# Kernel optimization log

Measured on AMD Instinct MI355X. Metric: run time of the kernel, lower is better.

Reference implementation:

```python
import jax, jax.numpy as jnp
import numpy as np

B, T, I, H, L, O = 256, 256, 512, 1024, 2, 1


def setup_inputs() -> dict:
    key = jax.random.key(0)
    ks = jax.random.split(key, 8)
    s_i = 1.0 / np.sqrt(I)
    s_h = 1.0 / np.sqrt(H)
    return {
        "init_hidden": jax.random.normal(ks[0], (B, H), jnp.float32),
        "context": jax.random.normal(ks[1], (B, T, I), jnp.float32),
        "W_ih0": jax.random.normal(ks[2], (4 * H, I), jnp.float32) * s_i,
        "W_hh0": jax.random.normal(ks[3], (4 * H, H), jnp.float32) * s_h,
        "b_ih0": jnp.zeros((4 * H,), jnp.float32),
        "b_hh0": jnp.zeros((4 * H,), jnp.float32),
        "W_ih1": jax.random.normal(ks[4], (4 * H, H), jnp.float32) * s_h,
        "W_hh1": jax.random.normal(ks[5], (4 * H, H), jnp.float32) * s_h,
        "b_ih1": jnp.zeros((4 * H,), jnp.float32),
        "b_hh1": jnp.zeros((4 * H,), jnp.float32),
        "W_ro": jax.random.normal(ks[6], (O, H), jnp.float32) * s_h,
        "b_ro": jnp.zeros((O,), jnp.float32),
    }


def _lstm_layer(x, h0, c0, W_ih, W_hh, b_ih, b_hh):
    """x: [B,T,Din] -> all hidden states [B,T,H]. PyTorch gate order i,f,g,o."""
    # Precompute input contribution for all timesteps (one big GEMM).
    xg = jnp.einsum('btd,gd->btg', x, W_ih) + b_ih + b_hh  # [B,T,4H]

    def step(carry, xg_t):
        h, c = carry
        gates = xg_t + h @ W_hh.T                          # [B,4H]
        i, f, g, o = jnp.split(gates, 4, axis=-1)
        i = jax.nn.sigmoid(i)
        f = jax.nn.sigmoid(f)
        g = jnp.tanh(g)
        o = jax.nn.sigmoid(o)
        c = f * c + i * g
        h = o * jnp.tanh(c)
        return (h, c), h

    (_, _), hs = jax.lax.scan(step, (h0, c0), jnp.swapaxes(xg, 0, 1))
    return jnp.swapaxes(hs, 0, 1)  # [B,T,H]


def reference(init_hidden, context, W_ih0, W_hh0, b_ih0, b_hh0,
              W_ih1, W_hh1, b_ih1, b_hh1, W_ro, b_ro):
    c0 = jnp.zeros((context.shape[0], H), context.dtype)
    # h0 for every layer is the same init_hidden (torch.stack of init_hidden).
    h1 = _lstm_layer(context, init_hidden, c0, W_ih0, W_hh0, b_ih0, b_hh0)
    h2 = _lstm_layer(h1, init_hidden, c0, W_ih1, W_hh1, b_ih1, b_hh1)
    # readout on last timestep -> [B, O]
    return h2[:, -1, :] @ W_ro.T + b_ro
```

## Files before the change

kernel.cpp:

```cpp
#include <hip/hip_runtime.h>
#include <hip/hip_bf16.h>

#define B_ 256
#define T_ 256
#define I_ 512
#define H_ 1024
#define CH 8
#define NCH 32

typedef _Float16 half8 __attribute__((ext_vector_type(8)));
typedef float floatx4 __attribute__((ext_vector_type(4)));


__global__ __launch_bounds__(256) void prep_w(
    _Float16* __restrict__ dst, const float* __restrict__ src, int K) {
  const int np = blockIdx.y;
  const int k = blockIdx.x * 256 + threadIdx.x;
  const int cc = np & 63, g = cc >> 4, j = cc & 15;
  const int orig = g * H_ + (np >> 6) * 16 + j;
  dst[(size_t)np * K + k] = (_Float16)src[(size_t)orig * K + k];
}

__global__ __launch_bounds__(256) void prep_bias(
    float* __restrict__ bs0, float* __restrict__ bs1,
    const float* __restrict__ bih0, const float* __restrict__ bhh0,
    const float* __restrict__ bih1, const float* __restrict__ bhh1) {
  const int np = blockIdx.x * 256 + threadIdx.x;
  const int cc = np & 63, g = cc >> 4, j = cc & 15;
  const int orig = g * H_ + (np >> 6) * 16 + j;
  bs0[np] = bih0[orig] + bhh0[orig];
  bs1[np] = bih1[orig] + bhh1[orig];
}

__global__ __launch_bounds__(256) void prep_state(
    const float* __restrict__ init, _Float16* __restrict__ h1s,
    _Float16* __restrict__ h2s, float* __restrict__ c0, float* __restrict__ c1) {
  const int idx = blockIdx.x * 256 + threadIdx.x;
  const float v = init[idx];
  h1s[B_ * H_ + idx] = (_Float16)v;
  h2s[B_ * H_ + idx] = (_Float16)v;
  c0[idx] = 0.f;
  c1[idx] = 0.f;
}

template<int KK, int AMODE>
__global__ __launch_bounds__(256, 2) void gemm_xg(
    const void* __restrict__ Ap, const _Float16* __restrict__ Bw,
    const float* __restrict__ bias, _Float16* __restrict__ out, int tbase) {
  constexpr int NST = KK / 64;
  __shared__ _Float16 As[2][128 * 72];
  __shared__ _Float16 Bs[2][128 * 72];
  const int tid = threadIdx.x;
  const int row0 = blockIdx.x * 128, col0 = blockIdx.y * 128;
  const int sr = tid >> 1, sc = (tid & 1) * 32;
  const int gr = row0 + sr;
  const size_t arow = (AMODE == 0)
      ? ((size_t)(gr & 255) * T_ + (size_t)tbase + (gr >> 8)) * I_
      : (size_t)gr * KK;
  const float*    af32 = (const float*)Ap + arow + sc;
  const _Float16* af16 = (const _Float16*)Ap + arow + sc;
  const _Float16* bsrc = Bw + (size_t)(col0 + sr) * KK + sc;

  const int w = tid >> 6, lane = tid & 63;
  const int wm = (w >> 1) * 64, wn = (w & 1) * 64;
  const int l15 = lane & 15, kg = (lane >> 4) * 8;
  floatx4 acc[4][4] = {};
  half8 ar[4], br[4];

  auto load_stage = [&](int ki) {
    const int k = ki * 64;
    #pragma unroll
    for (int c = 0; c < 4; ++c) {
      if (AMODE == 0) {
        float4 f0 = *(const float4*)(af32 + k + c * 8);
        float4 f1 = *(const float4*)(af32 + k + c * 8 + 4);
        half8 h;
        h[0] = (_Float16)f0.x; h[1] = (_Float16)f0.y;
        h[2] = (_Float16)f0.z; h[3] = (_Float16)f0.w;
        h[4] = (_Float16)f1.x; h[5] = (_Float16)f1.y;
        h[6] = (_Float16)f1.z; h[7] = (_Float16)f1.w;
        ar[c] = h;
      } else {
        ar[c] = *(const half8*)(af16 + k + c * 8);
      }
      br[c] = *(const half8*)(bsrc + k + c * 8);
    }
  };
  auto write_stage = [&](int buf) {
    #pragma unroll
    for (int c = 0; c < 4; ++c) *(half8*)(&As[buf][sr * 72 + sc + c * 8]) = ar[c];
    #pragma unroll
    for (int c = 0; c < 4; ++c) *(half8*)(&Bs[buf][sr * 72 + sc + c * 8]) = br[c];
  };

  load_stage(0); write_stage(0); __syncthreads();
  for (int ki = 0; ki < NST; ++ki) {
    const int cur = ki & 1;
    if (ki + 1 < NST) load_stage(ki + 1);
    #pragma unroll
    for (int ks = 0; ks < 2; ++ks) {
      half8 bf[4];
      #pragma unroll
      for (int n = 0; n < 4; ++n)
        bf[n] = *(const half8*)(&Bs[cur][(wn + 16 * n + l15) * 72 + ks * 32 + kg]);
      #pragma unroll
      for (int m = 0; m < 4; ++m) {
        half8 af = *(const half8*)(&As[cur][(wm + 16 * m + l15) * 72 + ks * 32 + kg]);
        #pragma unroll
        for (int n = 0; n < 4; ++n)
          acc[m][n] = __builtin_amdgcn_mfma_f32_16x16x32_f16(af, bf[n], acc[m][n], 0, 0, 0);
      }
    }
    if (ki + 1 < NST) write_stage(cur ^ 1);
    __syncthreads();
  }

  const int crow = (lane >> 4) * 4;
  #pragma unroll
  for (int n = 0; n < 4; ++n) {
    const int col = col0 + wn + 16 * n + l15;
    const float bv = bias[col];
    #pragma unroll
    for (int m = 0; m < 4; ++m) {
      const int rbase = row0 + wm + 16 * m + crow;
      #pragma unroll
      for (int r = 0; r < 4; ++r)
        out[(size_t)(rbase + r) * 4096 + col] = (_Float16)(acc[m][n][r] + bv);
    }
  }
}

__global__ __launch_bounds__(256, 2) void lstm_step(
    const _Float16* __restrict__ Wh0, const _Float16* __restrict__ Wh1,
    const _Float16* __restrict__ xg0, const _Float16* __restrict__ xg1,
    _Float16* __restrict__ h1s, _Float16* __restrict__ h2s,
    _Float16* __restrict__ h1chunk, float* __restrict__ c0buf,
    float* __restrict__ c1buf, float* __restrict__ hF, int t0, int t1, int ci) {
  const int layer = blockIdx.x >> 8;
  const int t = layer ? t1 : t0;
  if (t < 0) return;
  const int tb = blockIdx.x & 255;
  const int row0 = (tb >> 6) * 64;
  const int nb = tb & 63;
  const int col0 = nb * 64;
  const _Float16* __restrict__ Wh = layer ? Wh1 : Wh0;
  const _Float16* __restrict__ xg = (layer ? xg1 : xg0) + (size_t)ci * 256 * 4096;
  _Float16* __restrict__ hs = layer ? h2s : h1s;
  float* __restrict__ cbuf = layer ? c1buf : c0buf;
  const int rd = (t + 1) & 1, wr = t & 1;
  const _Float16* __restrict__ hin = hs + rd * (B_ * H_);

  __shared__ _Float16 lds[2 * (2 * 2 * 64 * 72)];
  _Float16* As = lds;
  _Float16* Bs = lds + 2 * 2 * 64 * 72;
  float* gl = (float*)lds;

  const int tid = threadIdx.x;
  const int sr = tid >> 2, kh_s = (tid >> 1) & 1, coff = (tid & 1) * 32;
  const _Float16* asrc = hin + (size_t)(row0 + sr) * H_ + kh_s * 512 + coff;
  const _Float16* bsrc = Wh + (size_t)(col0 + sr) * H_ + kh_s * 512 + coff;
  const int sdst = kh_s * (64 * 72) + sr * 72 + coff;

  const int w = tid >> 6, lane = tid & 63;
  const int rh = (w & 1) * 32, kh = w >> 1;
  const int l15 = lane & 15, kg = (lane >> 4) * 8;
  floatx4 acc[2][4] = {};
  half8 ar[4], br[4];

  auto load_stage = [&](int ki) {
    #pragma unroll
    for (int c = 0; c < 4; ++c) ar[c] = *(const half8*)(asrc + ki * 64 + c * 8);
    #pragma unroll
    for (int c = 0; c < 4; ++c) br[c] = *(const half8*)(bsrc + ki * 64 + c * 8);
  };
  auto write_stage = [&](int buf) {
    _Float16* dA = As + buf * (2 * 64 * 72) + sdst;
    _Float16* dB = Bs + buf * (2 * 64 * 72) + sdst;
    #pragma unroll
    for (int c = 0; c < 4; ++c) *(half8*)(dA + c * 8) = ar[c];
    #pragma unroll
    for (int c = 0; c < 4; ++c) *(half8*)(dB + c * 8) = br[c];
  };

  load_stage(0); write_stage(0); __syncthreads();
  for (int ki = 0; ki < 8; ++ki) {
    const int cur = ki & 1;
    if (ki < 7) load_stage(ki + 1);
    const _Float16* Ab = As + cur * (2 * 64 * 72) + kh * (64 * 72);
    const _Float16* Bb = Bs + cur * (2 * 64 * 72) + kh * (64 * 72);
    #pragma unroll
    for (int ks = 0; ks < 2; ++ks) {
      half8 bf[4];
      #pragma unroll
      for (int n = 0; n < 4; ++n)
        bf[n] = *(const half8*)(Bb + (16 * n + l15) * 72 + ks * 32 + kg);
      #pragma unroll
      for (int m = 0; m < 2; ++m) {
        half8 af = *(const half8*)(Ab + (rh + 16 * m + l15) * 72 + ks * 32 + kg);
        #pragma unroll
        for (int n = 0; n < 4; ++n)
          acc[m][n] = __builtin_amdgcn_mfma_f32_16x16x32_f16(af, bf[n], acc[m][n], 0, 0, 0);
      }
    }
    if (ki < 7) write_stage(cur ^ 1);
    __syncthreads();
  }

  const int crow = (lane >> 4) * 4;
  if (kh == 0) {
    #pragma unroll
    for (int m = 0; m < 2; ++m)
      #pragma unroll
      for (int n = 0; n < 4; ++n) {
        const int col = 16 * n + l15, rowl = rh + 16 * m + crow;
        #pragma unroll
        for (int r = 0; r < 4; ++r) gl[(rowl + r) * 68 + col] = acc[m][n][r];
      }
  }
  __syncthreads();
  if (kh == 1) {
    #pragma unroll
    for (int m = 0; m < 2; ++m)
      #pragma unroll
      for (int n = 0; n < 4; ++n) {
        const int col = 16 * n + l15, rowl = rh + 16 * m + crow;
        #pragma unroll
        for (int r = 0; r < 4; ++r) gl[(rowl + r) * 68 + col] += acc[m][n][r];
      }
  }
  __syncthreads();

  #pragma unroll
  for (int q = 0; q < 4; ++q) {
    const int idx = tid + q * 256;
    const int r = idx >> 4, j = idx & 15;
    const int brow = row0 + r;
    const int hu = nb * 16 + j;
    const _Float16* xr = xg + (size_t)brow * 4096 + col0;
    float gi = gl[r * 68 + j]          + (float)xr[j];
    float gf = gl[r * 68 + 16 + j]     + (float)xr[16 + j];
    float gg = gl[r * 68 + 32 + j]     + (float)xr[32 + j];
    float go = gl[r * 68 + 48 + j]     + (float)xr[48 + j];
    const float si = 1.f / (1.f + expf(-gi));
    const float sf = 1.f / (1.f + expf(-gf));
    const float so = 1.f / (1.f + expf(-go));
    const float tg = tanhf(gg);
    const float cp = cbuf[(size_t)brow * H_ + hu];
    const float cn = sf * cp + si * tg;
    const float hn = so * tanhf(cn);
    cbuf[(size_t)brow * H_ + hu] = cn;
    hs[wr * (B_ * H_) + (size_t)brow * H_ + hu] = (_Float16)hn;
    if (layer == 0)
      h1chunk[((size_t)ci * 256 + brow) * H_ + hu] = (_Float16)hn;
    else
      hF[(size_t)brow * H_ + hu] = hn;
  }
}

__global__ __launch_bounds__(256) void readout(
    const float* __restrict__ hF, const float* __restrict__ Wro,
    const float* __restrict__ bro, float* __restrict__ out) {
  const int b = blockIdx.x;
  const int tid = threadIdx.x;
  float p = 0.f;
  for (int h = tid; h < H_; h += 256) p += hF[(size_t)b * H_ + h] * Wro[h];
  #pragma unroll
  for (int off = 32; off; off >>= 1) p += __shfl_down(p, off, 64);
  __shared__ float red[4];
  if ((tid & 63) == 0) red[tid >> 6] = p;
  __syncthreads();
  if (tid == 0) out[b] = red[0] + red[1] + red[2] + red[3] + bro[0];
}

extern "C" void kernel_launch(void* const* d_in, const int* in_sizes, int n_in,
                              void* d_out, int out_size, void* d_ws, size_t ws_size,
                              hipStream_t stream) {
  const float* init_hidden = (const float*)d_in[0];
  const float* ctx   = (const float*)d_in[1];
  const float* W_ih0 = (const float*)d_in[2];
  const float* W_hh0 = (const float*)d_in[3];
  const float* b_ih0 = (const float*)d_in[4];
  const float* b_hh0 = (const float*)d_in[5];
  const float* W_ih1 = (const float*)d_in[6];
  const float* W_hh1 = (const float*)d_in[7];
  const float* b_ih1 = (const float*)d_in[8];
  const float* b_hh1 = (const float*)d_in[9];
  const float* W_ro  = (const float*)d_in[10];
  const float* b_ro  = (const float*)d_in[11];

  char* ws = (char*)d_ws;
  _Float16* W0p  = (_Float16*)(ws);
  _Float16* Wh0p = (_Float16*)(ws + 4194304);
  _Float16* W1p  = (_Float16*)(ws + 12582912);
  _Float16* Wh1p = (_Float16*)(ws + 20971520);
  float*    bs0  = (float*)(ws + 29360128);
  float*    bs1  = (float*)(ws + 29376512);
  _Float16* xg0  = (_Float16*)(ws + 29392896);
  _Float16* xg1  = (_Float16*)(ws + 46170112);
  _Float16* h1c  = (_Float16*)(ws + 62947328);
  _Float16* h1s  = (_Float16*)(ws + 67141632);
  _Float16* h2s  = (_Float16*)(ws + 68190208);
  float*    c0   = (float*)(ws + 69238784);
  float*    c1   = (float*)(ws + 70287360);
  float*    hF   = (float*)(ws + 71335936);

  prep_w<<<dim3(I_ / 256, 4096), 256, 0, stream>>>(W0p, W_ih0, I_);
  prep_w<<<dim3(H_ / 256, 4096), 256, 0, stream>>>(Wh0p, W_hh0, H_);
  prep_w<<<dim3(H_ / 256, 4096), 256, 0, stream>>>(W1p, W_ih1, H_);
  prep_w<<<dim3(H_ / 256, 4096), 256, 0, stream>>>(Wh1p, W_hh1, H_);
  prep_bias<<<dim3(16), 256, 0, stream>>>(bs0, bs1, b_ih0, b_hh0, b_ih1, b_hh1);
  prep_state<<<dim3(B_ * H_ / 256), 256, 0, stream>>>(init_hidden, h1s, h2s, c0, c1);

  for (int c = 0; c <= NCH; ++c) {
    if (c < NCH)
      gemm_xg<512, 0><<<dim3(16, 32), 256, 0, stream>>>(ctx, W0p, bs0, xg0, c * CH);
    if (c >= 1)
      gemm_xg<1024, 1><<<dim3(16, 32), 256, 0, stream>>>(h1c, W1p, bs1, xg1, 0);
    for (int i = 0; i < CH; ++i) {
      const int t0 = (c < NCH) ? c * CH + i : -1;
      const int t1 = (c >= 1) ? (c - 1) * CH + i : -1;
      lstm_step<<<dim3(512), 256, 0, stream>>>(Wh0p, Wh1p, xg0, xg1, h1s, h2s,
                                               h1c, c0, c1, hF, t0, t1, i);
    }
  }
  readout<<<dim3(B_), 256, 0, stream>>>(hF, W_ro, b_ro, (float*)d_out);
}
```

Baseline: 5.971 ms.

## Enlarge LSTM step tiles to full-K 128-row blocks and use fast activations

Measured after the change: 6.533 ms. 1.09x slower.

```diff
diff --git a/kernel.cpp b/kernel.cpp
--- a/kernel.cpp
+++ b/kernel.cpp
@@ -10,6 +10,13 @@
 
 typedef _Float16 half8 __attribute__((ext_vector_type(8)));
 typedef float floatx4 __attribute__((ext_vector_type(4)));
+
+__device__ __forceinline__ float fsig(float x) {
+  return 1.f / (1.f + __expf(-x));
+}
+__device__ __forceinline__ float ftanh(float x) {
+  return 1.f - 2.f / (__expf(2.f * x) + 1.f);
+}
 
 
 __global__ __launch_bounds__(256) void prep_w(
@@ -130,18 +137,19 @@
   }
 }
 
-__global__ __launch_bounds__(256, 2) void lstm_step(
+__global__ __launch_bounds__(256) void lstm_step(
     const _Float16* __restrict__ Wh0, const _Float16* __restrict__ Wh1,
     const _Float16* __restrict__ xg0, const _Float16* __restrict__ xg1,
     _Float16* __restrict__ h1s, _Float16* __restrict__ h2s,
     _Float16* __restrict__ h1chunk, float* __restrict__ c0buf,
     float* __restrict__ c1buf, float* __restrict__ hF, int t0, int t1, int ci) {
-  const int layer = blockIdx.x >> 8;
+  const int bid = blockIdx.x;
+  const int layer = bid >> 7;
   const int t = layer ? t1 : t0;
   if (t < 0) return;
-  const int tb = blockIdx.x & 255;
-  const int row0 = (tb >> 6) * 64;
-  const int nb = tb & 63;
+  const int b7 = bid & 127;
+  const int row0 = (b7 >> 6) * 128;
+  const int nb = b7 & 63;
   const int col0 = nb * 64;
   const _Float16* __restrict__ Wh = layer ? Wh1 : Wh0;
   const _Float16* __restrict__ xg = (layer ? xg1 : xg0) + (size_t)ci * 256 * 4096;
@@ -150,110 +158,83 @@
   const int rd = (t + 1) & 1, wr = t & 1;
   const _Float16* __restrict__ hin = hs + rd * (B_ * H_);
 
-  __shared__ _Float16 lds[2 * (2 * 2 * 64 * 72)];
-  _Float16* As = lds;
-  _Float16* Bs = lds + 2 * 2 * 64 * 72;
-  float* gl = (float*)lds;
+  __shared__ _Float16 As[2][128 * 72];
+  __shared__ _Float16 Bs[2][64 * 72];
 
   const int tid = threadIdx.x;
-  const int sr = tid >> 2, kh_s = (tid >> 1) & 1, coff = (tid & 1) * 32;
-  const _Float16* asrc = hin + (size_t)(row0 + sr) * H_ + kh_s * 512 + coff;
-  const _Float16* bsrc = Wh + (size_t)(col0 + sr) * H_ + kh_s * 512 + coff;
-  const int sdst = kh_s * (64 * 72) + sr * 72 + coff;
-
-  const int w = tid >> 6, lane = tid & 63;
-  const int rh = (w & 1) * 32, kh = w >> 1;
-  const int l15 = lane & 15, kg = (lane >> 4) * 8;
-  floatx4 acc[2][4] = {};
-  half8 ar[4], br[4];
+  const int srow = tid >> 3;
+  const int spc = (tid & 7) * 8;
+  const _Float16* asrc = hin + (size_t)(row0 + srow) * H_ + spc;
+  const _Float16* bsrc = Wh + (size_t)(col0 + srow) * H_ + spc;
+  half8 ar[4], br[2];
 
   auto load_stage = [&](int ki) {
-    #pragma unroll
-    for (int c = 0; c < 4; ++c) ar[c] = *(const half8*)(asrc + ki * 64 + c * 8);
-    #pragma unroll
-    for (int c = 0; c < 4; ++c) br[c] = *(const half8*)(bsrc + ki * 64 + c * 8);
+    const int k = ki * 64;
+    #pragma unroll
+    for (int p = 0; p < 4; ++p) ar[p] = *(const half8*)(asrc + (size_t)(p * 32) * H_ + k);
+    #pragma unroll
+    for (int p = 0; p < 2; ++p) br[p] = *(const half8*)(bsrc + (size_t)(p * 32) * H_ + k);
   };
   auto write_stage = [&](int buf) {
-    _Float16* dA = As + buf * (2 * 64 * 72) + sdst;
-    _Float16* dB = Bs + buf * (2 * 64 * 72) + sdst;
-    #pragma unroll
-    for (int c = 0; c < 4; ++c) *(half8*)(dA + c * 8) = ar[c];
-    #pragma unroll
-    for (int c = 0; c < 4; ++c) *(half8*)(dB + c * 8) = br[c];
+    #pragma unroll
+    for (int p = 0; p < 4; ++p) *(half8*)(&As[buf][(srow + p * 32) * 72 + spc]) = ar[p];
+    #pragma unroll
+    for (int p = 0; p < 2; ++p) *(half8*)(&Bs[buf][(srow + p * 32) * 72 + spc]) = br[p];
   };
 
+  const int w = tid >> 6, lane = tid & 63;
+  const int l15 = lane & 15, kg = (lane >> 4) * 8;
+  const int wrow = w * 32;
+  floatx4 acc[2][4] = {};
+
   load_stage(0); write_stage(0); __syncthreads();
-  for (int ki = 0; ki < 8; ++ki) {
+  for (int ki = 0; ki < 16; ++ki) {
     const int cur = ki & 1;
-    if (ki < 7) load_stage(ki + 1);
-    const _Float16* Ab = As + cur * (2 * 64 * 72) + kh * (64 * 72);
-    const _Float16* Bb = Bs + cur * (2 * 64 * 72) + kh * (64 * 72);
+    if (ki < 15) load_stage(ki + 1);
     #pragma unroll
     for (int ks = 0; ks < 2; ++ks) {
       half8 bf[4];
       #pragma unroll
       for (int n = 0; n < 4; ++n)
-        bf[n] = *(const half8*)(Bb + (16 * n + l15) * 72 + ks * 32 + kg);
+        bf[n] = *(const half8*)(&Bs[cur][(16 * n + l15) * 72 + ks * 32 + kg]);
       #pragma unroll
       for (int m = 0; m < 2; ++m) {
-        half8 af = *(const half8*)(Ab + (rh + 16 * m + l15) * 72 + ks * 32 + kg);
+        half8 af = *(const half8*)(&As[cur][(wrow + 16 * m + l15) * 72 + ks * 32 + kg]);
         #pragma unroll
         for (int n = 0; n < 4; ++n)
           acc[m][n] = __builtin_amdgcn_mfma_f32_16x16x32_f16(af, bf[n], acc[m][n], 0, 0, 0);
       }
     }
-    if (ki < 7) write_stage(cur ^ 1);
+    if (ki < 15) write_stage(cur ^ 1);
     __syncthreads();
   }
 
-  const int crow = (lane >> 4) * 4;
-  if (kh == 0) {
-    #pragma unroll
-    for (int m = 0; m < 2; ++m)
-      #pragma unroll
-      for (int n = 0; n < 4; ++n) {
-        const int col = 16 * n + l15, rowl = rh + 16 * m + crow;
-        #pragma unroll
-        for (int r = 0; r < 4; ++r) gl[(rowl + r) * 68 + col] = acc[m][n][r];
-      }
-  }
-  __syncthreads();
-  if (kh == 1) {
-    #pragma unroll
-    for (int m = 0; m < 2; ++m)
-      #pragma unroll
-      for (int n = 0; n < 4; ++n) {
-        const int col = 16 * n + l15, rowl = rh + 16 * m + crow;
-        #pragma unroll
-        for (int r = 0; r < 4; ++r) gl[(rowl + r) * 68 + col] += acc[m][n][r];
-      }
-  }
-  __syncthreads();
-
+  const int hu = nb * 16 + l15;
+  const int rsub = (lane >> 4) * 4;
   #pragma unroll
-  for (int q = 0; q < 4; ++q) {
-    const int idx = tid + q * 256;
-    const int r = idx >> 4, j = idx & 15;
-    const int brow = row0 + r;
-    const int hu = nb * 16 + j;
-    const _Float16* xr = xg + (size_t)brow * 4096 + col0;
-    float gi = gl[r * 68 + j]          + (float)xr[j];
-    float gf = gl[r * 68 + 16 + j]     + (float)xr[16 + j];
-    float gg = gl[r * 68 + 32 + j]     + (float)xr[32 + j];
-    float go = gl[r * 68 + 48 + j]     + (float)xr[48 + j];
-    const float si = 1.f / (1.f + expf(-gi));
-    const float sf = 1.f / (1.f + expf(-gf));
-    const float so = 1.f / (1.f + expf(-go));
-    const float tg = tanhf(gg);
-    const float cp = cbuf[(size_t)brow * H_ + hu];
-    const float cn = sf * cp + si * tg;
-    const float hn = so * tanhf(cn);
-    cbuf[(size_t)brow * H_ + hu] = cn;
-    hs[wr * (B_ * H_) + (size_t)brow * H_ + hu] = (_Float16)hn;
-    if (layer == 0)
-      h1chunk[((size_t)ci * 256 + brow) * H_ + hu] = (_Float16)hn;
-    else
-      hF[(size_t)brow * H_ + hu] = hn;
+  for (int m = 0; m < 2; ++m) {
+    #pragma unroll
+    for (int r = 0; r < 4; ++r) {
+      const int brow = row0 + wrow + 16 * m + rsub + r;
+      const _Float16* xr = xg + (size_t)brow * 4096 + col0;
+      const float gi = acc[m][0][r] + (float)xr[l15];
+      const float gf = acc[m][1][r] + (float)xr[16 + l15];
+      const float gg = acc[m][2][r] + (float)xr[32 + l15];
+      const float go = acc[m][3][r] + (float)xr[48 + l15];
+      const float si = fsig(gi);
+      const float sf = fsig(gf);
+      const float so = fsig(go);
+      const float tg = ftanh(gg);
+      const size_t cidx = (size_t)brow * H_ + hu;
+      const float cn = sf * cbuf[cidx] + si * tg;
+      const float hn = so * ftanh(cn);
+      cbuf[cidx] = cn;
+      hs[wr * (B_ * H_) + cidx] = (_Float16)hn;
+      if (layer == 0)
+        h1chunk[((size_t)ci * 256 + brow) * H_ + hu] = (_Float16)hn;
+      else
+        hF[cidx] = hn;
+    }
   }
 }
 
@@ -319,7 +300,7 @@
     for (int i = 0; i < CH; ++i) {
       const int t0 = (c < NCH) ? c * CH + i : -1;
       const int t1 = (c >= 1) ? (c - 1) * CH + i : -1;
-      lstm_step<<<dim3(512), 256, 0, stream>>>(Wh0p, Wh1p, xg0, xg1, h1s, h2s,
+      lstm_step<<<dim3(256), 256, 0, stream>>>(Wh0p, Wh1p, xg0, xg1, h1s, h2s,
                                                h1c, c0, c1, hF, t0, t1, i);
     }
   }
```
